# Optimization experiments

Measured on AMD Instinct MI355X. Metric: run time of the kernel, lower is better.

## Reference

```python
import jax, jax.numpy as jnp
import numpy as np

B, I, H, O, K = 4096, 512, 512, 512, 32

def _linear_params(key, out_dim, in_dim):
    kw, _ = jax.random.split(key)
    W = jax.random.normal(kw, (out_dim, in_dim), dtype=jnp.float32) / np.sqrt(in_dim)
    b = jnp.zeros((out_dim,), dtype=jnp.float32)
    return W, b

def setup_inputs() -> dict:
    key = jax.random.key(0)
    ks = jax.random.split(key, 9)
    sample = jax.random.normal(ks[0], (B, I), dtype=jnp.float32)
    hidden_state = jax.random.normal(ks[1], (B, H), dtype=jnp.float32)
    cell_tensors = jax.random.normal(ks[2], (K, B, H), dtype=jnp.float32)
    mem_para = 0.5 * jax.random.uniform(ks[3], (B, H), dtype=jnp.float32)
    W_i, b_i = _linear_params(ks[4], H, I + H)
    W_o, b_o = _linear_params(ks[5], H, I + H)
    W_m, b_m = _linear_params(ks[6], H, I + 2 * H)
    W_c, b_c = _linear_params(ks[7], H, I + H)
    W_out, b_out = _linear_params(ks[8], O, H)
    return {"sample": sample, "hidden_state": hidden_state,
            "cell_tensors": cell_tensors, "mem_para": mem_para,
            "W_i": W_i, "b_i": b_i, "W_o": W_o, "b_o": b_o,
            "W_m": W_m, "b_m": b_m, "W_c": W_c, "b_c": b_c,
            "W_out": W_out, "b_out": b_out}

def _mem_weights(mem_para, k):
    # weights[k-1-i] = prod_{j=0..i} (j - d)/(j+1)  -> cumprod then reverse
    i = jnp.arange(k, dtype=mem_para.dtype)[:, None, None]  # [k,1,1]
    factors = (i - mem_para[None]) / (i + 1.0)               # [k,B,H]
    return jnp.cumprod(factors, axis=0)[::-1]                # [k,B,H]

def reference(sample, hidden_state, cell_tensors, mem_para,
              W_i, b_i, W_o, b_o, W_m, b_m, W_c, b_c, W_out, b_out):
    k = cell_tensors.shape[0]
    xh = jnp.concatenate([sample, hidden_state], axis=1)            # [B, I+H]
    xhd = jnp.concatenate([sample, hidden_state, mem_para], axis=1)  # [B, I+2H]
    i_gate = jax.nn.sigmoid(xh @ W_i.T + b_i)
    o_gate = jax.nn.sigmoid(xh @ W_o.T + b_o)
    mem_new = 0.5 * jax.nn.sigmoid(xhd @ W_m.T + b_m)
    c_tilde = jnp.tanh(xh @ W_c.T + b_c)
    w = _mem_weights(mem_new, k)                                     # [k,B,H]
    cell_filtered = -(cell_tensors * w).sum(axis=0)                  # [B,H]
    cell_new = cell_filtered + c_tilde * i_gate
    updated_cell_states = jnp.concatenate([cell_tensors[1:], cell_new[None]], axis=0)
    hidden_new = o_gate * jnp.tanh(cell_new)
    output = hidden_new @ W_out.T + b_out
    return (output, hidden_new, updated_cell_states, mem_new)
```

## Files before the change

### kernel.cpp

```cpp
#include <hip/hip_runtime.h>

typedef __attribute__((ext_vector_type(8))) short short8;
typedef __attribute__((ext_vector_type(4))) short sh4;
typedef __attribute__((ext_vector_type(4))) float f32x4;

#define BH 2097152
#define NK 32

static __device__ __forceinline__ short f2bf(float f) {
  union { float f; unsigned int u; } c; c.f = f;
  unsigned int u = c.u + 0x7FFFu + ((c.u >> 16) & 1u);
  return (short)(u >> 16);
}
static __device__ __forceinline__ float bf2f(short s) {
  union { unsigned int u; float f; } c;
  c.u = ((unsigned int)(unsigned short)s) << 16;
  return c.f;
}
static __device__ __forceinline__ f32x4 ntload(const float* p) {
  return __builtin_nontemporal_load((const f32x4*)p);
}
static __device__ __forceinline__ void ntstore(float* p, f32x4 v) {
  __builtin_nontemporal_store(v, (f32x4*)p);
}

#define WS_XH     0
#define WS_MEMPB  4194304
#define WS_WI     6291456
#define WS_WO     6815744
#define WS_WC     7340032
#define WS_WM     7864320
#define WS_WOUT   8650752
#define WS_HIDB   8912896
#define WS_IGB    11010048
#define WS_OGB    13107200
#define WS_CGB    15204352
#define WS_END    17301504
#define FAST_NEED_BYTES ((size_t)WS_END * 2)


__global__ __launch_bounds__(256) void prep(
    const float* __restrict__ sample, const float* __restrict__ hidden,
    const float* __restrict__ memp,
    const float* __restrict__ wi, const float* __restrict__ wo,
    const float* __restrict__ wc, const float* __restrict__ wm,
    const float* __restrict__ wout, short* __restrict__ ws) {
  const size_t v = ((size_t)blockIdx.x * 256 + threadIdx.x) * 4;
  const float* src;
  short* dst;
  if (v < 2097152) {
    const size_t r = v >> 9, c = v & 511;
    src = sample + v; dst = ws + WS_XH + r * 1024 + c;
  } else if (v < 4194304) {
    const size_t u = v - 2097152, r = u >> 9, c = u & 511;
    src = hidden + u; dst = ws + WS_XH + r * 1024 + 512 + c;
  } else if (v < 6291456) {
    const size_t u = v - 4194304; src = memp + u; dst = ws + WS_MEMPB + u;
  } else if (v < 6815744) {
    const size_t u = v - 6291456; src = wi + u; dst = ws + WS_WI + u;
  } else if (v < 7340032) {
    const size_t u = v - 6815744; src = wo + u; dst = ws + WS_WO + u;
  } else if (v < 7864320) {
    const size_t u = v - 7340032; src = wc + u; dst = ws + WS_WC + u;
  } else if (v < 8650752) {
    const size_t u = v - 7864320; src = wm + u; dst = ws + WS_WM + u;
  } else {
    const size_t u = v - 8650752; src = wout + u; dst = ws + WS_WOUT + u;
  }
  const f32x4 x = *(const f32x4*)src;
  sh4 s;
#pragma unroll
  for (int j = 0; j < 4; ++j) s[j] = f2bf(x[j]);
  *(sh4*)dst = s;
}

struct FastArgs {
  const short *xh, *mempb, *hidb;
  const short *W[5];
  const float *bia[5];
  short *gdst[3];
  float *memo, *out0;
};

__global__ __launch_bounds__(256) void gemm_fast(FastArgs a, int mode) {
  __shared__ short lA[2][64 * 64];
  __shared__ short lB[2][64 * 64];
  const int t = threadIdx.x;
  const int lane = t & 63;
  const int wv = t >> 6;
  const int mt = blockIdx.x;
  int gate, nsub;
  if (mode == 0) {
    const int gmap[4] = {3, 0, 1, 2};
    gate = gmap[blockIdx.y >> 3]; nsub = blockIdx.y & 7;
  } else { gate = 4; nsub = blockIdx.y; }
  const short* W = a.W[gate];
  const int Klen = (gate == 3) ? 1536 : (gate == 4 ? 512 : 1024);
  const int m0 = mt * 64;
  const int n0 = nsub * 64;

  f32x4 acc[2][2];
  const f32x4 z = {0.f, 0.f, 0.f, 0.f};
#pragma unroll
  for (int i = 0; i < 2; ++i)
#pragma unroll
    for (int j = 0; j < 2; ++j) acc[i][j] = z;

  const int wr = wv >> 1, wc2 = wv & 1;

  auto stage = [&](int buf, int kt) {
    const int kb = kt << 6;
#pragma unroll
    for (int it = 0; it < 2; ++it) {
      const int chunk = it * 256 + t;
      const int row = chunk >> 3;
      const int kk = (chunk & 7) << 3;
      const int gk = kb + kk;
      const short* src;
      if (gate == 4)                    src = a.hidb  + (size_t)(m0 + row) * 512 + gk;
      else if (gate != 3 || gk < 1024)  src = a.xh    + (size_t)(m0 + row) * 1024 + gk;
      else                              src = a.mempb + (size_t)(m0 + row) * 512 + (gk - 1024);
      __builtin_amdgcn_global_load_lds(
          (const __attribute__((address_space(1))) void*)src,
          (__attribute__((address_space(3))) void*)(&lA[buf][0] + (size_t)(it * 256 + wv * 64) * 8),
          16, 0, 0);
    }
#pragma unroll
    for (int it = 0; it < 2; ++it) {
      const int chunk = it * 256 + t;
      const int row = chunk >> 3;
      const int kk = (chunk & 7) << 3;
      const short* src = W + (size_t)(n0 + row) * Klen + kb + kk;
      __builtin_amdgcn_global_load_lds(
          (const __attribute__((address_space(1))) void*)src,
          (__attribute__((address_space(3))) void*)(&lB[buf][0] + (size_t)(it * 256 + wv * 64) * 8),
          16, 0, 0);
    }
  };

  const int Ktiles = Klen >> 6;
  stage(0, 0);
  __syncthreads();
  int cur = 0;
  for (int kt = 0; kt < Ktiles; ++kt) {
    if (kt + 1 < Ktiles) stage(cur ^ 1, kt + 1);
#pragma unroll
    for (int ks = 0; ks < 2; ++ks) {
      short8 av[2], bv[2];
#pragma unroll
      for (int mi = 0; mi < 2; ++mi)
        av[mi] = *(const short8*)(&lA[cur][0] + (wr * 32 + mi * 16 + (lane & 15)) * 64 + ks * 32 + ((lane >> 4) << 3));
#pragma unroll
      for (int ni = 0; ni < 2; ++ni)
        bv[ni] = *(const short8*)(&lB[cur][0] + (wc2 * 32 + ni * 16 + (lane & 15)) * 64 + ks * 32 + ((lane >> 4) << 3));
#pragma unroll
      for (int mi = 0; mi < 2; ++mi)
#pragma unroll
        for (int ni = 0; ni < 2; ++ni)
          acc[mi][ni] = __builtin_amdgcn_mfma_f32_16x16x32_bf16(av[mi], bv[ni], acc[mi][ni], 0, 0, 0);
    }
    __syncthreads();
    cur ^= 1;
  }

  const float* bias = a.bia[gate];
  const int rg = lane >> 4;
  const int ci = lane & 15;
#pragma unroll
  for (int mi = 0; mi < 2; ++mi) {
#pragma unroll
    for (int ni = 0; ni < 2; ++ni) {
      const int col = n0 + wc2 * 32 + ni * 16 + ci;
      const float bvl = bias[col];
#pragma unroll
      for (int r = 0; r < 4; ++r) {
        const int row = m0 + wr * 32 + mi * 16 + rg * 4 + r;
        const float v = acc[mi][ni][r] + bvl;
        const size_t o = (size_t)row * 512 + col;
        if (gate == 0)      a.gdst[0][o] = f2bf(1.f / (1.f + __expf(-v)));
        else if (gate == 1) a.gdst[1][o] = f2bf(1.f / (1.f + __expf(-v)));
        else if (gate == 2) a.gdst[2][o] = f2bf(1.f - 2.f / (1.f + __expf(2.f * v)));
        else if (gate == 3) a.memo[o] = 0.5f / (1.f + __expf(-v));
        else                a.out0[o] = v;
      }
    }
  }
}

__global__ __launch_bounds__(256, 8) void cell_update_b(
    const float* __restrict__ cell, const short* __restrict__ igb,
    const short* __restrict__ ogb, const short* __restrict__ cgb,
    const float* __restrict__ mem, float* __restrict__ upd,
    float* __restrict__ hid, short* __restrict__ hidb)
{
  const size_t idx = ((size_t)blockIdx.x * 256 + threadIdx.x) * 4;
  const f32x4 dv = *(const f32x4*)(mem + idx);
  const sh4 iv = *(const sh4*)(igb + idx);
  const sh4 ov = *(const sh4*)(ogb + idx);
  const sh4 gv = *(const sh4*)(cgb + idx);
  float p[4], acc[4];
#pragma unroll
  for (int j = 0; j < 4; ++j) { p[j] = 1.f; acc[j] = 0.f; }
#pragma unroll
  for (int i = 0; i < 32; ++i) {
    const int k = 31 - i;
    const f32x4 c = ntload(cell + (size_t)k * BH + idx);
    const float inv = 1.f / (float)(i + 1);
#pragma unroll
    for (int j = 0; j < 4; ++j) {
      p[j] *= ((float)i - dv[j]) * inv;
      acc[j] += c[j] * p[j];
    }
    if (k >= 1) ntstore(upd + (size_t)(k - 1) * BH + idx, c);
  }
  f32x4 cno, ho; sh4 hb;
#pragma unroll
  for (int j = 0; j < 4; ++j) {
    const float cn = -acc[j] + bf2f(gv[j]) * bf2f(iv[j]);
    cno[j] = cn;
    const float th = 1.f - 2.f / (1.f + __expf(2.f * cn));
    const float h = bf2f(ov[j]) * th;
    ho[j] = h; hb[j] = f2bf(h);
  }
  ntstore(upd + (size_t)31 * BH + idx, cno);
  *(f32x4*)(hid + idx) = ho;
  *(sh4*)(hidb + idx) = hb;
}


struct GemmArgs {
  const float *sample, *hidden, *memp, *hid_in;
  const float *W[5];
  const float *bia[5];
  float *dst[5];
};

__global__ __launch_bounds__(256) void gemm_all(GemmArgs g, int mode) {
  __shared__ short lA[128 * 64];
  __shared__ short lB[128 * 64];
  const int t = threadIdx.x;
  const int lane = t & 63;
  const int mt = blockIdx.x;
  int gate, nsub;
  if (mode == 0) { gate = blockIdx.y >> 2; nsub = blockIdx.y & 3; }
  else           { gate = 4;               nsub = blockIdx.y; }
  const float* W = g.W[gate];
  const float* bias = g.bia[gate];
  float* dst = g.dst[gate];
  const int Klen = (gate == 3) ? 1536 : (gate == 4 ? 512 : 1024);
  const int m0 = mt * 128;
  const int n0 = nsub * 128;

  f32x4 acc[4][4];
  const f32x4 z = {0.f, 0.f, 0.f, 0.f};
#pragma unroll
  for (int i = 0; i < 4; ++i)
#pragma unroll
    for (int j = 0; j < 4; ++j) acc[i][j] = z;

  const int wv = t >> 6;
  const int wr = wv >> 1, wc = wv & 1;
  const int Ktiles = Klen >> 6;
  for (int kt = 0; kt < Ktiles; ++kt) {
    const int kb = kt << 6;
#pragma unroll
    for (int it = 0; it < 4; ++it) {
      const int chunk = it * 256 + t;
      const int row = chunk >> 3;
      const int kk = (chunk & 7) << 3;
      const int gk = kb + kk;
      const float* src;
      if (mode == 1)      src = g.hid_in + (size_t)(m0 + row) * 512 + gk;
      else if (gk < 512)  src = g.sample + (size_t)(m0 + row) * 512 + gk;
      else if (gk < 1024) src = g.hidden + (size_t)(m0 + row) * 512 + (gk - 512);
      else                src = g.memp   + (size_t)(m0 + row) * 512 + (gk - 1024);
      const f32x4 v0 = *(const f32x4*)src;
      const f32x4 v1 = *(const f32x4*)(src + 4);
      short8 s;
#pragma unroll
      for (int j = 0; j < 4; ++j) { s[j] = f2bf(v0[j]); s[4 + j] = f2bf(v1[j]); }
      *(short8*)(lA + row * 64 + kk) = s;
    }
#pragma unroll
    for (int it = 0; it < 4; ++it) {
      const int chunk = it * 256 + t;
      const int row = chunk >> 3;
      const int kk = (chunk & 7) << 3;
      const float* src = W + (size_t)(n0 + row) * Klen + kb + kk;
      const f32x4 v0 = *(const f32x4*)src;
      const f32x4 v1 = *(const f32x4*)(src + 4);
      short8 s;
#pragma unroll
      for (int j = 0; j < 4; ++j) { s[j] = f2bf(v0[j]); s[4 + j] = f2bf(v1[j]); }
      *(short8*)(lB + row * 64 + kk) = s;
    }
    __syncthreads();
#pragma unroll
    for (int ks = 0; ks < 2; ++ks) {
      short8 av[4], bv[4];
#pragma unroll
      for (int mi = 0; mi < 4; ++mi)
        av[mi] = *(const short8*)(lA + (wr * 64 + mi * 16 + (lane & 15)) * 64 + ks * 32 + ((lane >> 4) << 3));
#pragma unroll
      for (int ni = 0; ni < 4; ++ni)
        bv[ni] = *(const short8*)(lB + (wc * 64 + ni * 16 + (lane & 15)) * 64 + ks * 32 + ((lane >> 4) << 3));
#pragma unroll
      for (int mi = 0; mi < 4; ++mi)
#pragma unroll
        for (int ni = 0; ni < 4; ++ni)
          acc[mi][ni] = __builtin_amdgcn_mfma_f32_16x16x32_bf16(av[mi], bv[ni], acc[mi][ni], 0, 0, 0);
    }
    __syncthreads();
  }

  const int rg = lane >> 4;
  const int ci = lane & 15;
#pragma unroll
  for (int mi = 0; mi < 4; ++mi) {
#pragma unroll
    for (int ni = 0; ni < 4; ++ni) {
      const int col = n0 + wc * 64 + ni * 16 + ci;
      const float bvl = bias[col];
#pragma unroll
      for (int r = 0; r < 4; ++r) {
        const int row = m0 + wr * 64 + mi * 16 + rg * 4 + r;
        const float v = acc[mi][ni][r] + bvl;
        float o;
        if (gate == 0 || gate == 1)  o = 1.f / (1.f + __expf(-v));
        else if (gate == 2)          o = 1.f - 2.f / (1.f + __expf(2.f * v));
        else if (gate == 3)          o = 0.5f / (1.f + __expf(-v));
        else                         o = v;
        dst[(size_t)row * 512 + col] = o;
      }
    }
  }
}

__global__ __launch_bounds__(256) void cell_update(
    const float* __restrict__ cell, const float* ig, const float* og, const float* cg,
    const float* mem, float* upd, float* __restrict__ hid)
{
  const size_t idx = ((size_t)blockIdx.x * 256 + threadIdx.x) * 4;
  const f32x4 dv = *(const f32x4*)(mem + idx);
  const f32x4 iv = *(const f32x4*)(ig + idx);
  const f32x4 ov = *(const f32x4*)(og + idx);
  const f32x4 gv = *(const f32x4*)(cg + idx);
  asm volatile("" ::: "memory");
  float p[4], acc[4];
#pragma unroll
  for (int j = 0; j < 4; ++j) { p[j] = 1.f; acc[j] = 0.f; }
#pragma unroll
  for (int i = 0; i < 32; ++i) {
    const int k = 31 - i;
    const f32x4 c = *(const f32x4*)(cell + (size_t)k * BH + idx);
    const float inv = 1.f / (float)(i + 1);
#pragma unroll
    for (int j = 0; j < 4; ++j) {
      p[j] *= ((float)i - dv[j]) * inv;
      acc[j] += c[j] * p[j];
    }
    if (k >= 1) *(f32x4*)(upd + (size_t)(k - 1) * BH + idx) = c;
  }
  f32x4 cno, ho;
#pragma unroll
  for (int j = 0; j < 4; ++j) {
    const float cn = -acc[j] + gv[j] * iv[j];
    cno[j] = cn;
    const float th = 1.f - 2.f / (1.f + __expf(2.f * cn));
    ho[j] = ov[j] * th;
  }
  *(f32x4*)(upd + (size_t)31 * BH + idx) = cno;
  *(f32x4*)(hid + idx) = ho;
}


extern "C" void kernel_launch(void* const* d_in, const int* in_sizes, int n_in,
                              void* d_out, int out_size, void* d_ws, size_t ws_size,
                              hipStream_t stream) {
  const float* sample = (const float*)d_in[0];
  const float* hidden = (const float*)d_in[1];
  const float* cell   = (const float*)d_in[2];
  const float* memp   = (const float*)d_in[3];

  float* out0 = (float*)d_out;
  float* hid  = out0 + (size_t)BH;
  float* upd  = hid + (size_t)BH;
  float* memo = upd + (size_t)NK * BH;

  if (ws_size >= FAST_NEED_BYTES) {
    short* ws = (short*)d_ws;
    hipLaunchKernelGGL(prep, dim3(8704), dim3(256), 0, stream,
                       sample, hidden, memp,
                       (const float*)d_in[4], (const float*)d_in[6],
                       (const float*)d_in[10], (const float*)d_in[8],
                       (const float*)d_in[12], ws);
    FastArgs a;
    a.xh = ws + WS_XH; a.mempb = ws + WS_MEMPB; a.hidb = ws + WS_HIDB;
    a.W[0] = ws + WS_WI; a.W[1] = ws + WS_WO; a.W[2] = ws + WS_WC;
    a.W[3] = ws + WS_WM; a.W[4] = ws + WS_WOUT;
    a.bia[0] = (const float*)d_in[5];  a.bia[1] = (const float*)d_in[7];
    a.bia[2] = (const float*)d_in[11]; a.bia[3] = (const float*)d_in[9];
    a.bia[4] = (const float*)d_in[13];
    a.gdst[0] = ws + WS_IGB; a.gdst[1] = ws + WS_OGB; a.gdst[2] = ws + WS_CGB;
    a.memo = memo; a.out0 = out0;

    hipLaunchKernelGGL(gemm_fast, dim3(64, 32), dim3(256), 0, stream, a, 0);
    hipLaunchKernelGGL(cell_update_b, dim3(2048), dim3(256), 0, stream,
                       cell, (const short*)a.gdst[0], (const short*)a.gdst[1],
                       (const short*)a.gdst[2], (const float*)memo, upd, hid,
                       ws + WS_HIDB);
    hipLaunchKernelGGL(gemm_fast, dim3(64, 8), dim3(256), 0, stream, a, 1);
    return;
  }

  float* ig;
  float* og;
  float* cg;
  if (ws_size >= (size_t)3 * BH * sizeof(float)) {
    ig = (float*)d_ws; og = ig + (size_t)BH; cg = og + (size_t)BH;
  } else {
    ig = upd; og = upd + (size_t)BH; cg = upd + 2 * (size_t)BH;
  }
  GemmArgs g;
  g.sample = sample; g.hidden = hidden; g.memp = memp; g.hid_in = hid;
  g.W[0] = (const float*)d_in[4];  g.bia[0] = (const float*)d_in[5];
  g.W[1] = (const float*)d_in[6];  g.bia[1] = (const float*)d_in[7];
  g.W[3] = (const float*)d_in[8];  g.bia[3] = (const float*)d_in[9];
  g.W[2] = (const float*)d_in[10]; g.bia[2] = (const float*)d_in[11];
  g.W[4] = (const float*)d_in[12]; g.bia[4] = (const float*)d_in[13];
  g.dst[0] = ig; g.dst[1] = og; g.dst[2] = cg; g.dst[3] = memo; g.dst[4] = out0;

  hipLaunchKernelGGL(gemm_all, dim3(32, 16), dim3(256), 0, stream, g, 0);
  hipLaunchKernelGGL(cell_update, dim3(2048), dim3(256), 0, stream,
                     cell, (const float*)ig, (const float*)og, (const float*)cg,
                     (const float*)memo, upd, hid);
  hipLaunchKernelGGL(gemm_all, dim3(32, 4), dim3(256), 0, stream, g, 1);
}
```

Baseline: 185.4 us.

## Fuse gate GEMMs with cell-history streaming into a single mega kernel

The i/o/c gate GEMMs are folded into a new kernel that keeps the activated gates in registers and then streams the 32-step cell history for the same 64x64 tile, computing the new cell and hidden state in place. The separate bf16 gate buffers and the cell_update launch go away, and the mem-gate GEMM is split into its own launch. Blocks alternate between doing GEMM first and streaming first, so compute and memory phases overlap across the GPU. The trade-off is that the streaming now runs on only 512 blocks using scalar per-element loads and stores, which may reduce memory-level parallelism and coalescing.

```diff
diff --git a/kernel.cpp b/kernel.cpp
--- a/kernel.cpp
+++ b/kernel.cpp
@@ -17,10 +17,16 @@
   c.u = ((unsigned int)(unsigned short)s) << 16;
   return c.f;
 }
-static __device__ __forceinline__ f32x4 ntload(const float* p) {
+static __device__ __forceinline__ float ntloadf(const float* p) {
+  return __builtin_nontemporal_load(p);
+}
+static __device__ __forceinline__ void ntstoref(float* p, float v) {
+  __builtin_nontemporal_store(v, p);
+}
+static __device__ __forceinline__ f32x4 ntload4(const float* p) {
   return __builtin_nontemporal_load((const f32x4*)p);
 }
-static __device__ __forceinline__ void ntstore(float* p, f32x4 v) {
+static __device__ __forceinline__ void ntstore4(float* p, f32x4 v) {
   __builtin_nontemporal_store(v, (f32x4*)p);
 }
 
@@ -78,7 +84,6 @@
   const short *xh, *mempb, *hidb;
   const short *W[5];
   const float *bia[5];
-  short *gdst[3];
   float *memo, *out0;
 };
 
@@ -89,13 +94,10 @@
   const int lane = t & 63;
   const int wv = t >> 6;
   const int mt = blockIdx.x;
-  int gate, nsub;
-  if (mode == 0) {
-    const int gmap[4] = {3, 0, 1, 2};
-    gate = gmap[blockIdx.y >> 3]; nsub = blockIdx.y & 7;
-  } else { gate = 4; nsub = blockIdx.y; }
+  const int gate = (mode == 2) ? 3 : 4;
+  const int nsub = blockIdx.y;
   const short* W = a.W[gate];
-  const int Klen = (gate == 3) ? 1536 : (gate == 4 ? 512 : 1024);
+  const int Klen = (gate == 3) ? 1536 : 512;
   const int m0 = mt * 64;
   const int n0 = nsub * 64;
 
@@ -117,9 +119,9 @@
       const int kk = (chunk & 7) << 3;
       const int gk = kb + kk;
       const short* src;
-      if (gate == 4)                    src = a.hidb  + (size_t)(m0 + row) * 512 + gk;
-      else if (gate != 3 || gk < 1024)  src = a.xh    + (size_t)(m0 + row) * 1024 + gk;
-      else                              src = a.mempb + (size_t)(m0 + row) * 512 + (gk - 1024);
+      if (gate == 4)       src = a.hidb  + (size_t)(m0 + row) * 512 + gk;
+      else if (gk < 1024)  src = a.xh    + (size_t)(m0 + row) * 1024 + gk;
+      else                 src = a.mempb + (size_t)(m0 + row) * 512 + (gk - 1024);
       __builtin_amdgcn_global_load_lds(
           (const __attribute__((address_space(1))) void*)src,
           (__attribute__((address_space(3))) void*)(&lA[buf][0] + (size_t)(it * 256 + wv * 64) * 8),
@@ -177,54 +179,173 @@
         const int row = m0 + wr * 32 + mi * 16 + rg * 4 + r;
         const float v = acc[mi][ni][r] + bvl;
         const size_t o = (size_t)row * 512 + col;
-        if (gate == 0)      a.gdst[0][o] = f2bf(1.f / (1.f + __expf(-v)));
-        else if (gate == 1) a.gdst[1][o] = f2bf(1.f / (1.f + __expf(-v)));
-        else if (gate == 2) a.gdst[2][o] = f2bf(1.f - 2.f / (1.f + __expf(2.f * v)));
-        else if (gate == 3) a.memo[o] = 0.5f / (1.f + __expf(-v));
-        else                a.out0[o] = v;
+        if (gate == 3) a.memo[o] = 0.5f / (1.f + __expf(-v));
+        else           a.out0[o] = v;
       }
     }
   }
 }
 
-__global__ __launch_bounds__(256, 8) void cell_update_b(
-    const float* __restrict__ cell, const short* __restrict__ igb,
-    const short* __restrict__ ogb, const short* __restrict__ cgb,
-    const float* __restrict__ mem, float* __restrict__ upd,
-    float* __restrict__ hid, short* __restrict__ hidb)
+__global__ __launch_bounds__(256) void mega(
+    FastArgs a, const float* __restrict__ cell, const float* __restrict__ mem,
+    float* __restrict__ upd, float* __restrict__ hid, short* __restrict__ hidb)
 {
-  const size_t idx = ((size_t)blockIdx.x * 256 + threadIdx.x) * 4;
-  const f32x4 dv = *(const f32x4*)(mem + idx);
-  const sh4 iv = *(const sh4*)(igb + idx);
-  const sh4 ov = *(const sh4*)(ogb + idx);
-  const sh4 gv = *(const sh4*)(cgb + idx);
-  float p[4], acc[4];
-#pragma unroll
-  for (int j = 0; j < 4; ++j) { p[j] = 1.f; acc[j] = 0.f; }
-#pragma unroll
-  for (int i = 0; i < 32; ++i) {
-    const int k = 31 - i;
-    const f32x4 c = ntload(cell + (size_t)k * BH + idx);
-    const float inv = 1.f / (float)(i + 1);
-#pragma unroll
-    for (int j = 0; j < 4; ++j) {
-      p[j] *= ((float)i - dv[j]) * inv;
-      acc[j] += c[j] * p[j];
-    }
-    if (k >= 1) ntstore(upd + (size_t)(k - 1) * BH + idx, c);
-  }
-  f32x4 cno, ho; sh4 hb;
-#pragma unroll
-  for (int j = 0; j < 4; ++j) {
-    const float cn = -acc[j] + bf2f(gv[j]) * bf2f(iv[j]);
-    cno[j] = cn;
-    const float th = 1.f - 2.f / (1.f + __expf(2.f * cn));
-    const float h = bf2f(ov[j]) * th;
-    ho[j] = h; hb[j] = f2bf(h);
-  }
-  ntstore(upd + (size_t)31 * BH + idx, cno);
-  *(f32x4*)(hid + idx) = ho;
-  *(sh4*)(hidb + idx) = hb;
+  __shared__ short lA[2][64 * 64];
+  __shared__ short lB[2][64 * 64];
+  const int t = threadIdx.x;
+  const int lane = t & 63;
+  const int wv = t >> 6;
+  const int mt = blockIdx.x;
+  const int nsub = blockIdx.y;
+  const int m0 = mt * 64;
+  const int n0 = nsub * 64;
+  const int wr = wv >> 1, wc2 = wv & 1;
+  const int rg = lane >> 4, ci = lane & 15;
+
+  float g3[3][2][2][4];
+  float ac[2][2][4];
+  unsigned idxv[2][2][4];
+#pragma unroll
+  for (int mi = 0; mi < 2; ++mi)
+#pragma unroll
+    for (int ni = 0; ni < 2; ++ni)
+#pragma unroll
+      for (int r = 0; r < 4; ++r) {
+        const int row = m0 + wr * 32 + mi * 16 + rg * 4 + r;
+        const int col = n0 + wc2 * 32 + ni * 16 + ci;
+        idxv[mi][ni][r] = (unsigned)(row * 512 + col);
+      }
+
+  auto phaseG = [&]() {
+#pragma unroll
+    for (int g = 0; g < 3; ++g) {
+      const short* W = a.W[g];
+      f32x4 acc[2][2];
+      const f32x4 z = {0.f, 0.f, 0.f, 0.f};
+#pragma unroll
+      for (int i = 0; i < 2; ++i)
+#pragma unroll
+        for (int j = 0; j < 2; ++j) acc[i][j] = z;
+
+      auto stage = [&](int buf, int kt) {
+        const int kb = kt << 6;
+#pragma unroll
+        for (int it = 0; it < 2; ++it) {
+          const int chunk = it * 256 + t;
+          const int row = chunk >> 3;
+          const int kk = (chunk & 7) << 3;
+          const short* src = a.xh + (size_t)(m0 + row) * 1024 + kb + kk;
+          __builtin_amdgcn_global_load_lds(
+              (const __attribute__((address_space(1))) void*)src,
+              (__attribute__((address_space(3))) void*)(&lA[buf][0] + (size_t)(it * 256 + wv * 64) * 8),
+              16, 0, 0);
+        }
+#pragma unroll
+        for (int it = 0; it < 2; ++it) {
+          const int chunk = it * 256 + t;
+          const int row = chunk >> 3;
+          const int kk = (chunk & 7) << 3;
+          const short* src = W + (size_t)(n0 + row) * 1024 + kb + kk;
+          __builtin_amdgcn_global_load_lds(
+              (const __attribute__((address_space(1))) void*)src,
+              (__attribute__((address_space(3))) void*)(&lB[buf][0] + (size_t)(it * 256 + wv * 64) * 8),
+              16, 0, 0);
+        }
+      };
+
+      stage(0, 0);
+      __syncthreads();
+      int cur = 0;
+      for (int kt = 0; kt < 16; ++kt) {
+        if (kt + 1 < 16) stage(cur ^ 1, kt + 1);
+#pragma unroll
+        for (int ks = 0; ks < 2; ++ks) {
+          short8 av[2], bv[2];
+#pragma unroll
+          for (int mi = 0; mi < 2; ++mi)
+            av[mi] = *(const short8*)(&lA[cur][0] + (wr * 32 + mi * 16 + (lane & 15)) * 64 + ks * 32 + ((lane >> 4) << 3));
+#pragma unroll
+          for (int ni = 0; ni < 2; ++ni)
+            bv[ni] = *(const short8*)(&lB[cur][0] + (wc2 * 32 + ni * 16 + (lane & 15)) * 64 + ks * 32 + ((lane >> 4) << 3));
+#pragma unroll
+          for (int mi = 0; mi < 2; ++mi)
+#pragma unroll
+            for (int ni = 0; ni < 2; ++ni)
+              acc[mi][ni] = __builtin_amdgcn_mfma_f32_16x16x32_bf16(av[mi], bv[ni], acc[mi][ni], 0, 0, 0);
+        }
+        __syncthreads();
+        cur ^= 1;
+      }
+
+      const float* bias = a.bia[g];
+#pragma unroll
+      for (int mi = 0; mi < 2; ++mi)
+#pragma unroll
+        for (int ni = 0; ni < 2; ++ni) {
+          const int col = n0 + wc2 * 32 + ni * 16 + ci;
+          const float bvl = bias[col];
+#pragma unroll
+          for (int r = 0; r < 4; ++r) {
+            const float v = acc[mi][ni][r] + bvl;
+            if (g == 2) g3[2][mi][ni][r] = 1.f - 2.f / (1.f + __expf(2.f * v));
+            else        g3[g][mi][ni][r] = 1.f / (1.f + __expf(-v));
+          }
+        }
+    }
+  };
+
+  auto phaseS = [&]() {
+    float d[2][2][4], pp[2][2][4];
+#pragma unroll
+    for (int mi = 0; mi < 2; ++mi)
+#pragma unroll
+      for (int ni = 0; ni < 2; ++ni)
+#pragma unroll
+        for (int r = 0; r < 4; ++r) {
+          d[mi][ni][r] = mem[idxv[mi][ni][r]];
+          pp[mi][ni][r] = 1.f;
+          ac[mi][ni][r] = 0.f;
+        }
+#pragma unroll
+    for (int i2 = 0; i2 < 32; ++i2) {
+      const int k = 31 - i2;
+      const float inv = 1.f / (float)(i2 + 1);
+      const float* cp = cell + (size_t)k * BH;
+      float* up = upd + (size_t)(k - 1) * BH;
+#pragma unroll
+      for (int mi = 0; mi < 2; ++mi)
+#pragma unroll
+        for (int ni = 0; ni < 2; ++ni)
+#pragma unroll
+          for (int r = 0; r < 4; ++r) {
+            const unsigned ix = idxv[mi][ni][r];
+            const float cv = ntloadf(cp + ix);
+            pp[mi][ni][r] *= ((float)i2 - d[mi][ni][r]) * inv;
+            ac[mi][ni][r] += cv * pp[mi][ni][r];
+            if (k >= 1) ntstoref(up + ix, cv);
+          }
+    }
+  };
+
+  const int par = (mt + nsub) & 1;
+  if (par == 0) { phaseG(); phaseS(); }
+  else          { phaseS(); phaseG(); }
+
+  float* up31 = upd + (size_t)31 * BH;
+#pragma unroll
+  for (int mi = 0; mi < 2; ++mi)
+#pragma unroll
+    for (int ni = 0; ni < 2; ++ni)
+#pragma unroll
+      for (int r = 0; r < 4; ++r) {
+        const unsigned ix = idxv[mi][ni][r];
+        const float cn = -ac[mi][ni][r] + g3[2][mi][ni][r] * g3[0][mi][ni][r];
+        ntstoref(up31 + ix, cn);
+        const float th = 1.f - 2.f / (1.f + __expf(2.f * cn));
+        const float h = g3[1][mi][ni][r] * th;
+        hid[ix] = h;
+        hidb[ix] = f2bf(h);
+      }
 }
 
 
@@ -401,14 +522,11 @@
     a.bia[0] = (const float*)d_in[5];  a.bia[1] = (const float*)d_in[7];
     a.bia[2] = (const float*)d_in[11]; a.bia[3] = (const float*)d_in[9];
     a.bia[4] = (const float*)d_in[13];
-    a.gdst[0] = ws + WS_IGB; a.gdst[1] = ws + WS_OGB; a.gdst[2] = ws + WS_CGB;
     a.memo = memo; a.out0 = out0;
 
-    hipLaunchKernelGGL(gemm_fast, dim3(64, 32), dim3(256), 0, stream, a, 0);
-    hipLaunchKernelGGL(cell_update_b, dim3(2048), dim3(256), 0, stream,
-                       cell, (const short*)a.gdst[0], (const short*)a.gdst[1],
-                       (const short*)a.gdst[2], (const float*)memo, upd, hid,
-                       ws + WS_HIDB);
+    hipLaunchKernelGGL(gemm_fast, dim3(64, 8), dim3(256), 0, stream, a, 2);
+    hipLaunchKernelGGL(mega, dim3(64, 8), dim3(256), 0, stream,
+                       a, cell, (const float*)memo, upd, hid, ws + WS_HIDB);
     hipLaunchKernelGGL(gemm_fast, dim3(64, 8), dim3(256), 0, stream, a, 1);
     return;
   }
```

New measurement: 538.9 us. 191% more time.
